# Optimization experiments

Measured on AMD Instinct MI355X. Metric: run time of the kernel, lower is better.

Reference implementation:

```python
import jax, jax.numpy as jnp
import numpy as np

BN_EPS = 1e-5


def scatter_mean(src, idx, num_segments):
    # torch_scatter scatter_mean: sum / clamp(count, min=1)
    s = jax.ops.segment_sum(src, idx, num_segments=num_segments)
    c = jax.ops.segment_sum(jnp.ones((src.shape[0],), src.dtype), idx, num_segments=num_segments)
    return s / jnp.maximum(c, 1.0)[:, None]


def batch_norm(h, gamma, beta):
    # BatchNorm1d with track_running_stats=False: always uses batch stats (biased var)
    mu = jnp.mean(h, axis=0, keepdims=True)
    var = jnp.mean((h - mu) ** 2, axis=0, keepdims=True)
    return (h - mu) * jax.lax.rsqrt(var + BN_EPS) * gamma + beta


def setup_inputs() -> dict:
    key = jax.random.key(0)
    ks = jax.random.split(key, 16)
    N, E, B, D = 50000, 800000, 256, 64
    x = jax.random.normal(ks[0], (N, D), dtype=jnp.float32)
    edge_attr = jax.random.normal(ks[1], (E, D), dtype=jnp.float32)
    u = jax.random.normal(ks[2], (B, D), dtype=jnp.float32)
    edge_index = jax.random.randint(ks[3], (2, E), 0, N, dtype=jnp.int64)
    batch = jnp.sort(jax.random.randint(ks[4], (N,), 0, B, dtype=jnp.int64))
    def lin_init(k, fan_in, fan_out):
        k1, k2 = jax.random.split(k)
        bound = 1.0 / np.sqrt(fan_in)
        W = jax.random.uniform(k1, (fan_out, fan_in), minval=-bound, maxval=bound, dtype=jnp.float32)
        b = jax.random.uniform(k2, (fan_out,), minval=-bound, maxval=bound, dtype=jnp.float32)
        return W, b
    W0, b0 = lin_init(ks[5], 3 * D, D)
    W1, b1 = lin_init(ks[6], D, D)
    W2, b2 = lin_init(ks[7], D, D)
    g0 = jnp.ones((D,), jnp.float32); be0 = jnp.zeros((D,), jnp.float32)
    g1 = jnp.ones((D,), jnp.float32); be1 = jnp.zeros((D,), jnp.float32)
    g2 = jnp.ones((D,), jnp.float32); be2 = jnp.zeros((D,), jnp.float32)
    return dict(x=x, edge_attr=edge_attr, u=u, edge_index=edge_index, batch=batch,
                W0=W0, b0=b0, W1=W1, b1=b1, W2=W2, b2=b2,
                g0=g0, be0=be0, g1=g1, be1=be1, g2=g2, be2=be2)


def reference(x, edge_attr, u, edge_index, batch,
              W0, b0, W1, b1, W2, b2, g0, be0, g1, be1, g2, be2):
    N = x.shape[0]
    B = u.shape[0]
    # edge -> node mean, then node -> graph mean
    u_e = scatter_mean(edge_attr, edge_index[0, :], N)   # [N, D]
    u_e = scatter_mean(u_e, batch, B)                    # [B, D]
    u_v = scatter_mean(x, batch, B)                      # [B, D]
    comb = jnp.concatenate([u_e, u_v, u], axis=1)        # [B, 3D]
    out = comb
    for (W, b, g, be) in ((W0, b0, g0, be0), (W1, b1, g1, be1), (W2, b2, g2, be2)):
        out = out @ W.T + b
        out = jax.nn.relu(out)
        out = batch_norm(out, g, be)
        # dropout is a no-op in eval mode
    return out
```

## Files before the change

kernel.cpp:

```cpp
#include <hip/hip_runtime.h>
#include <hip/hip_bf16.h>

#define DD 64
#define ECH 128
#define NEB 256
#define GB 256
#define MAXPER 3200

typedef __attribute__((ext_vector_type(8))) short bf16x8_t;
typedef __attribute__((ext_vector_type(4))) float f32x4_t;

__device__ __forceinline__ ushort f2b(float x) {
  __hip_bfloat16 h = __float2bfloat16(x);
  ushort r;
  __builtin_memcpy(&r, &h, 2);
  return r;
}

__device__ __forceinline__ uint swz(uint b) { return b ^ ((((b >> 8) & 7u)) << 4); }

__global__ __launch_bounds__(256) void k_zero(int* __restrict__ p, int n) {
  int gid = blockIdx.x * blockDim.x + threadIdx.x;
  int stride = gridDim.x * blockDim.x;
  for (int i = gid; i < n; i += stride) p[i] = 0;
}

__global__ __launch_bounds__(256) void k_hist(const int* __restrict__ eidx,
                                              int* __restrict__ cnt, int E) {
  int gid = blockIdx.x * blockDim.x + threadIdx.x;
  int stride = gridDim.x * blockDim.x;
  int E4 = E >> 2;
  const int4* e4 = reinterpret_cast<const int4*>(eidx);
  for (int i = gid; i < E4; i += stride) {
    int4 v = e4[i];
    atomicAdd(&cnt[v.x], 1);
    atomicAdd(&cnt[v.y], 1);
    atomicAdd(&cnt[v.z], 1);
    atomicAdd(&cnt[v.w], 1);
  }
  for (int e = (E4 << 2) + gid; e < E; e += stride) atomicAdd(&cnt[eidx[e]], 1);
}

__global__ __launch_bounds__(512) void k_edgesum(const float* __restrict__ edge_attr,
                                                 const int* __restrict__ eidx,
                                                 const int* __restrict__ cnt,
                                                 const int* __restrict__ batch,
                                                 float* __restrict__ partial, int E) {
  __shared__ ushort S[256 * 128];
  __shared__ ushort Vt[64 * 128];
  __shared__ int2 meta[MAXPER];
  const int tid = threadIdx.x;
  const int lane = tid & 63, wv = tid >> 6;
  const int r15 = lane & 15, kq = lane >> 4;

  const int per = (E + NEB - 1) / NEB;
  const int base = blockIdx.x * per;
  const int nE = max(0, min(per, E - base));
  const int nch = (nE + ECH - 1) / ECH;

  const int e0 = (tid >> 3) * 2;
  const int d0 = (tid & 7) * 8;

  float4 rA[4], rB[4];

#define LOADC(c, R)                                                              \
  do {                                                                           \
    size_t r0_ = (size_t)min(base + (c)*ECH + e0, E - 1);                        \
    size_t r1_ = (size_t)min(base + (c)*ECH + e0 + 1, E - 1);                    \
    const float4* p0_ = reinterpret_cast<const float4*>(edge_attr + r0_ * DD + d0); \
    const float4* p1_ = reinterpret_cast<const float4*>(edge_attr + r1_ * DD + d0); \
    R[0] = p0_[0];                                                               \
    R[1] = p0_[1];                                                               \
    R[2] = p1_[0];                                                               \
    R[3] = p1_[1];                                                               \
  } while (0)

#define PHASEW(c, R)                                                             \
  do {                                                                           \
    _Pragma("unroll") for (int q = 0; q < 2; ++q) {                              \
      _Pragma("unroll") for (int j = 0; j < 4; ++j) {                            \
        int d_ = d0 + q * 4 + j;                                                 \
        uint w32_ = (uint)f2b(((const float*)&R[q])[j]) |                        \
                    ((uint)f2b(((const float*)&R[2 + q])[j]) << 16);             \
        *(uint*)((char*)Vt + swz(((uint)d_ * 128 + e0) * 2)) = w32_;             \
      }                                                                          \
    }                                                                            \
    if (tid < ECH) {                                                             \
      if (prev >= 0) *(ushort*)((char*)S + swz(((uint)prev * 128 + tid) * 2)) = 0; \
      int2 mm_ = meta[(c)*ECH + tid];                                            \
      if (mm_.x >= 0) {                                                          \
        *(ushort*)((char*)S + swz(((uint)mm_.x * 128 + tid) * 2)) =              \
            f2b(__int_as_float(mm_.y));                                          \
        prev = mm_.x;                                                            \
      } else {                                                                   \
        prev = -1;                                                               \
      }                                                                          \
    }                                                                            \
  } while (0)

#define MFMAP()                                                                  \
  do {                                                                           \
    _Pragma("unroll") for (int ks = 0; ks < 4; ++ks) {                           \
      uint ko_ = (uint)(ks * 32 + kq * 8) * 2;                                   \
      bf16x8_t a0_ = *(const bf16x8_t*)((const char*)S +                         \
                                        swz((uint)(wv * 32 + r15) * 256 + ko_)); \
      bf16x8_t a1_ = *(const bf16x8_t*)((const char*)S +                         \
                                        swz((uint)(wv * 32 + 16 + r15) * 256 + ko_)); \
      bf16x8_t b0_ = *(const bf16x8_t*)((const char*)Vt + swz((uint)(r15)*256 + ko_)); \
      bf16x8_t b1_ = *(const bf16x8_t*)((const char*)Vt +                        \
                                        swz((uint)(16 + r15) * 256 + ko_));      \
      bf16x8_t b2_ = *(const bf16x8_t*)((const char*)Vt +                        \
                                        swz((uint)(32 + r15) * 256 + ko_));      \
      bf16x8_t b3_ = *(const bf16x8_t*)((const char*)Vt +                        \
                                        swz((uint)(48 + r15) * 256 + ko_));      \
      acc[0][0] = __builtin_amdgcn_mfma_f32_16x16x32_bf16(a0_, b0_, acc[0][0], 0, 0, 0); \
      acc[0][1] = __builtin_amdgcn_mfma_f32_16x16x32_bf16(a0_, b1_, acc[0][1], 0, 0, 0); \
      acc[0][2] = __builtin_amdgcn_mfma_f32_16x16x32_bf16(a0_, b2_, acc[0][2], 0, 0, 0); \
      acc[0][3] = __builtin_amdgcn_mfma_f32_16x16x32_bf16(a0_, b3_, acc[0][3], 0, 0, 0); \
      acc[1][0] = __builtin_amdgcn_mfma_f32_16x16x32_bf16(a1_, b0_, acc[1][0], 0, 0, 0); \
      acc[1][1] = __builtin_amdgcn_mfma_f32_16x16x32_bf16(a1_, b1_, acc[1][1], 0, 0, 0); \
      acc[1][2] = __builtin_amdgcn_mfma_f32_16x16x32_bf16(a1_, b2_, acc[1][2], 0, 0, 0); \
      acc[1][3] = __builtin_amdgcn_mfma_f32_16x16x32_bf16(a1_, b3_, acc[1][3], 0, 0, 0); \
    }                                                                            \
  } while (0)

#define LGKM0() asm volatile("s_waitcnt lgkmcnt(0)" ::: "memory")

  f32x4_t acc[2][4];
#pragma unroll
  for (int a = 0; a < 2; ++a)
#pragma unroll
    for (int nt = 0; nt < 4; ++nt) acc[a][nt] = (f32x4_t)(0.0f);

  LOADC(0, rA);
  if (nch > 1) LOADC(1, rB);
  for (int i = tid; i < 256 * 128 / 2; i += 512) ((uint*)S)[i] = 0u;
  for (int i = tid; i < MAXPER; i += 512) {
    int pb = -1;
    float pw = 0.f;
    if (i < nE) {
      int n = eidx[base + i];
      pw = 1.0f / fmaxf((float)cnt[n], 1.0f);
      pb = batch[n];
    }
    meta[i] = make_int2(pb, __float_as_int(pw));
  }
  int prev = -1;
  __syncthreads();

  for (int c = 0; c < nch; c += 2) {
    PHASEW(c, rA);
    LGKM0();
    __builtin_amdgcn_s_barrier();
    if (c + 2 < nch) LOADC(c + 2, rA);
    MFMAP();
    LGKM0();
    __builtin_amdgcn_s_barrier();
    if (c + 1 < nch) {
      PHASEW(c + 1, rB);
      LGKM0();
      __builtin_amdgcn_s_barrier();
      if (c + 3 < nch) LOADC(c + 3, rB);
      MFMAP();
      LGKM0();
      __builtin_amdgcn_s_barrier();
    }
  }

  float* outp = partial + (size_t)blockIdx.x * GB * DD;
#pragma unroll
  for (int a = 0; a < 2; ++a)
#pragma unroll
    for (int nt = 0; nt < 4; ++nt)
#pragma unroll
      for (int j = 0; j < 4; ++j) {
        int row = wv * 32 + a * 16 + kq * 4 + j;
        int col = nt * 16 + r15;
        outp[row * DD + col] = acc[a][nt][j];
      }
#undef LOADC
#undef PHASEW
#undef MFMAP
#undef LGKM0
}

__global__ __launch_bounds__(256) void k_reduce(const float* __restrict__ partial,
                                                const float* __restrict__ x,
                                                const float* __restrict__ u,
                                                const int* __restrict__ batch,
                                                ushort* __restrict__ comb, int N) {
  __shared__ int s_lo, s_hi;
  __shared__ float rE[4][64], rV[4][64];
  int b = blockIdx.x;
  int tid = threadIdx.x;
  if (tid == 0) {
    int lo = 0, hi = N;
    while (lo < hi) { int m = (lo + hi) >> 1; if (batch[m] < b) lo = m + 1; else hi = m; }
    s_lo = lo;
    hi = N;
    while (lo < hi) { int m = (lo + hi) >> 1; if (batch[m] < b + 1) lo = m + 1; else hi = m; }
    s_hi = lo;
  }
  __syncthreads();
  int lo = s_lo, hi = s_hi;
  int d = tid & 63, sub = tid >> 6;
  float accE = 0.f, accV = 0.f;
  for (int p = sub; p < NEB; p += 4)
    accE += partial[((size_t)p * GB + b) * DD + d];
  for (int n = lo + sub; n < hi; n += 4)
    accV += x[(size_t)n * DD + d];
  rE[sub][d] = accE;
  rV[sub][d] = accV;
  __syncthreads();
  if (sub == 0) {
    float invNb = 1.0f / fmaxf((float)(hi - lo), 1.0f);
    float ue = (rE[0][d] + rE[1][d] + rE[2][d] + rE[3][d]) * invNb;
    float uv = (rV[0][d] + rV[1][d] + rV[2][d] + rV[3][d]) * invNb;
    ushort* row = comb + (size_t)b * 192;
    row[d] = f2b(ue);
    row[64 + d] = f2b(uv);
    row[128 + d] = f2b(u[(size_t)b * DD + d]);
  }
}

template <int K, int WS, bool FIRST, bool LAST>
__device__ __forceinline__ void mlp_layer(int tid, const ushort* __restrict__ combg,
                                          float* hbuf, ushort* a_lds,
                                          const ushort* w_lds, const float* bias_s,
                                          float* ps, float* pq, float* ab, float* bb,
                                          const float* __restrict__ gamma,
                                          const float* __restrict__ beta,
                                          float* __restrict__ out) {
  const int lane = tid & 63, wv = tid >> 6;
  f32x4_t acc[2][4];
#pragma unroll
  for (int a = 0; a < 2; ++a)
#pragma unroll
    for (int nt = 0; nt < 4; ++nt) acc[a][nt] = (f32x4_t)(0.0f);

  const int m0 = wv * 32;
  const int r15 = lane & 15, kq = lane >> 4;
  for (int kk = 0; kk < K; kk += 32) {
    int koff = kk + kq * 8;
    bf16x8_t af[2], bf[4];
    if (FIRST) {
      const ushort* ap = combg + (size_t)(m0 + r15) * 192 + koff;
      af[0] = *reinterpret_cast<const bf16x8_t*>(ap);
      af[1] = *reinterpret_cast<const bf16x8_t*>(ap + 16 * 192);
    } else {
      const ushort* ap = &a_lds[(m0 + r15) * 72 + koff];
      af[0] = *reinterpret_cast<const bf16x8_t*>(ap);
      af[1] = *reinterpret_cast<const bf16x8_t*>(ap + 16 * 72);
    }
#pragma unroll
    for (int nt = 0; nt < 4; ++nt)
      bf[nt] = *reinterpret_cast<const bf16x8_t*>(&w_lds[(nt * 16 + r15) * WS + koff]);
#pragma unroll
    for (int a = 0; a < 2; ++a)
#pragma unroll
      for (int nt = 0; nt < 4; ++nt)
        acc[a][nt] = __builtin_amdgcn_mfma_f32_16x16x32_bf16(af[a], bf[nt], acc[a][nt], 0, 0, 0);
  }

#pragma unroll
  for (int a = 0; a < 2; ++a) {
#pragma unroll
    for (int nt = 0; nt < 4; ++nt) {
      int col = nt * 16 + r15;
#pragma unroll
      for (int j = 0; j < 4; ++j) {
        int row = m0 + a * 16 + kq * 4 + j;
        float v = acc[a][nt][j] + bias_s[col];
        hbuf[row * 65 + col] = fmaxf(v, 0.f);
      }
    }
  }
  __syncthreads();

  {
    int col = tid & 63, seg = tid >> 6;
    float s = 0.f, q = 0.f;
#pragma unroll
    for (int t = 0; t < 32; ++t) {
      float v = hbuf[(seg * 32 + t) * 65 + col];
      s += v;
      q += v * v;
    }
    ps[seg * 64 + col] = s;
    pq[seg * 64 + col] = q;
  }
  __syncthreads();
  if (tid < 64) {
    float s = 0.f, q = 0.f;
#pragma unroll
    for (int g = 0; g < 8; ++g) {
      s += ps[g * 64 + tid];
      q += pq[g * 64 + tid];
    }
    float mu = s * (1.0f / 256.0f);
    float var = q * (1.0f / 256.0f) - mu * mu;
    float rs = rsqrtf(var + 1e-5f);
    float A = gamma[tid] * rs;
    ab[tid] = A;
    bb[tid] = beta[tid] - mu * A;
  }
  __syncthreads();
  for (int i = tid; i < 256 * 64; i += 512) {
    int r = i >> 6, c = i & 63;
    float y = hbuf[r * 65 + c] * ab[c] + bb[c];
    if (LAST)
      out[i] = y;
    else
      a_lds[r * 72 + c] = f2b(y);
  }
  __syncthreads();
}

__global__ __launch_bounds__(512) void k_mlp(const ushort* __restrict__ comb,
                                             const float* W0, const float* b0,
                                             const float* W1, const float* b1,
                                             const float* W2, const float* b2,
                                             const float* g0, const float* be0,
                                             const float* g1, const float* be1,
                                             const float* g2, const float* be2,
                                             float* __restrict__ out) {
  __shared__ __align__(16) float hbuf[256 * 65];
  __shared__ __align__(16) ushort a_lds[256 * 72];
  __shared__ __align__(16) ushort w0s[64 * 200];
  __shared__ __align__(16) ushort w1s[64 * 72];
  __shared__ __align__(16) ushort w2s[64 * 72];
  __shared__ float ps[8 * 64], pq[8 * 64];
  __shared__ float b0s[64], b1s[64], b2s[64], ab[64], bb[64];
  int tid = threadIdx.x;

  for (int i = tid; i < 64 * 192; i += 512) {
    int r = i / 192, c = i - r * 192;
    w0s[r * 200 + c] = f2b(W0[i]);
  }
  for (int i = tid; i < 64 * 64; i += 512) {
    int r = i >> 6, c = i & 63;
    w1s[r * 72 + c] = f2b(W1[i]);
    w2s[r * 72 + c] = f2b(W2[i]);
  }
  if (tid < 64) {
    b0s[tid] = b0[tid];
    b1s[tid] = b1[tid];
    b2s[tid] = b2[tid];
  }
  __syncthreads();

  mlp_layer<192, 200, true, false>(tid, comb, hbuf, a_lds, w0s, b0s, ps, pq, ab, bb,
                                   g0, be0, nullptr);
  mlp_layer<64, 72, false, false>(tid, comb, hbuf, a_lds, w1s, b1s, ps, pq, ab, bb,
                                  g1, be1, nullptr);
  mlp_layer<64, 72, false, true>(tid, comb, hbuf, a_lds, w2s, b2s, ps, pq, ab, bb,
                                 g2, be2, out);
}

extern "C" void kernel_launch(void* const* d_in, const int* in_sizes, int n_in,
                              void* d_out, int out_size, void* d_ws, size_t ws_size,
                              hipStream_t stream) {
  (void)n_in; (void)out_size; (void)ws_size;
  const float* x         = (const float*)d_in[0];
  const float* edge_attr = (const float*)d_in[1];
  const float* u         = (const float*)d_in[2];
  const int*   eidx      = (const int*)d_in[3];
  const int*   batch     = (const int*)d_in[4];
  const float* W0 = (const float*)d_in[5];
  const float* b0 = (const float*)d_in[6];
  const float* W1 = (const float*)d_in[7];
  const float* b1 = (const float*)d_in[8];
  const float* W2 = (const float*)d_in[9];
  const float* b2 = (const float*)d_in[10];
  const float* g0 = (const float*)d_in[11];
  const float* be0 = (const float*)d_in[12];
  const float* g1 = (const float*)d_in[13];
  const float* be1 = (const float*)d_in[14];
  const float* g2 = (const float*)d_in[15];
  const float* be2 = (const float*)d_in[16];

  int N = in_sizes[0] / DD;
  int E = in_sizes[1] / DD;

  float* partial = (float*)d_ws;
  int* cnt = (int*)(partial + (size_t)NEB * GB * DD);
  ushort* comb = (ushort*)(cnt + ((N + 3) & ~3));

  k_zero<<<64, 256, 0, stream>>>(cnt, N);
  k_hist<<<1024, 256, 0, stream>>>(eidx, cnt, E);
  k_edgesum<<<NEB, 512, 0, stream>>>(edge_attr, eidx, cnt, batch, partial, E);
  k_reduce<<<256, 256, 0, stream>>>(partial, x, u, batch, comb, N);
  k_mlp<<<1, 512, 0, stream>>>(comb, W0, b0, W1, b1, W2, b2,
                               g0, be0, g1, be1, g2, be2, (float*)d_out);
}
```

Before: 143.0 us.

## Split MFMA K-dimension across wave halves and widen swizzle to cut LDS traffic

```diff
diff --git a/kernel.cpp b/kernel.cpp
--- a/kernel.cpp
+++ b/kernel.cpp
@@ -17,7 +17,9 @@
   return r;
 }
 
-__device__ __forceinline__ uint swz(uint b) { return b ^ ((((b >> 8) & 7u)) << 4); }
+__device__ __forceinline__ uint swz(uint b) {
+  return b ^ (((((b >> 8) & 7u)) ^ ((b >> 11) & 7u)) << 4);
+}
 
 __global__ __launch_bounds__(256) void k_zero(int* __restrict__ p, int n) {
   int gid = blockIdx.x * blockDim.x + threadIdx.x;
@@ -52,6 +54,8 @@
   const int tid = threadIdx.x;
   const int lane = tid & 63, wv = tid >> 6;
   const int r15 = lane & 15, kq = lane >> 4;
+  const int kh = wv >> 2;
+  const int mq = wv & 3;
 
   const int per = (E + NEB - 1) / NEB;
   const int base = blockIdx.x * per;
@@ -100,12 +104,8 @@
 
 #define MFMAP()                                                                  \
   do {                                                                           \
-    _Pragma("unroll") for (int ks = 0; ks < 4; ++ks) {                           \
-      uint ko_ = (uint)(ks * 32 + kq * 8) * 2;                                   \
-      bf16x8_t a0_ = *(const bf16x8_t*)((const char*)S +                         \
-                                        swz((uint)(wv * 32 + r15) * 256 + ko_)); \
-      bf16x8_t a1_ = *(const bf16x8_t*)((const char*)S +                         \
-                                        swz((uint)(wv * 32 + 16 + r15) * 256 + ko_)); \
+    _Pragma("unroll") for (int ks = 0; ks < 2; ++ks) {                           \
+      uint ko_ = (uint)((kh * 2 + ks) * 32 + kq * 8) * 2;                        \
       bf16x8_t b0_ = *(const bf16x8_t*)((const char*)Vt + swz((uint)(r15)*256 + ko_)); \
       bf16x8_t b1_ = *(const bf16x8_t*)((const char*)Vt +                        \
                                         swz((uint)(16 + r15) * 256 + ko_));      \
@@ -113,22 +113,22 @@
                                         swz((uint)(32 + r15) * 256 + ko_));      \
       bf16x8_t b3_ = *(const bf16x8_t*)((const char*)Vt +                        \
                                         swz((uint)(48 + r15) * 256 + ko_));      \
-      acc[0][0] = __builtin_amdgcn_mfma_f32_16x16x32_bf16(a0_, b0_, acc[0][0], 0, 0, 0); \
-      acc[0][1] = __builtin_amdgcn_mfma_f32_16x16x32_bf16(a0_, b1_, acc[0][1], 0, 0, 0); \
-      acc[0][2] = __builtin_amdgcn_mfma_f32_16x16x32_bf16(a0_, b2_, acc[0][2], 0, 0, 0); \
-      acc[0][3] = __builtin_amdgcn_mfma_f32_16x16x32_bf16(a0_, b3_, acc[0][3], 0, 0, 0); \
-      acc[1][0] = __builtin_amdgcn_mfma_f32_16x16x32_bf16(a1_, b0_, acc[1][0], 0, 0, 0); \
-      acc[1][1] = __builtin_amdgcn_mfma_f32_16x16x32_bf16(a1_, b1_, acc[1][1], 0, 0, 0); \
-      acc[1][2] = __builtin_amdgcn_mfma_f32_16x16x32_bf16(a1_, b2_, acc[1][2], 0, 0, 0); \
-      acc[1][3] = __builtin_amdgcn_mfma_f32_16x16x32_bf16(a1_, b3_, acc[1][3], 0, 0, 0); \
+      _Pragma("unroll") for (int mt = 0; mt < 4; ++mt) {                         \
+        bf16x8_t a_ = *(const bf16x8_t*)((const char*)S +                        \
+                                         swz((uint)(mq * 64 + mt * 16 + r15) * 256 + ko_)); \
+        acc[mt][0] = __builtin_amdgcn_mfma_f32_16x16x32_bf16(a_, b0_, acc[mt][0], 0, 0, 0); \
+        acc[mt][1] = __builtin_amdgcn_mfma_f32_16x16x32_bf16(a_, b1_, acc[mt][1], 0, 0, 0); \
+        acc[mt][2] = __builtin_amdgcn_mfma_f32_16x16x32_bf16(a_, b2_, acc[mt][2], 0, 0, 0); \
+        acc[mt][3] = __builtin_amdgcn_mfma_f32_16x16x32_bf16(a_, b3_, acc[mt][3], 0, 0, 0); \
+      }                                                                          \
     }                                                                            \
   } while (0)
 
 #define LGKM0() asm volatile("s_waitcnt lgkmcnt(0)" ::: "memory")
 
-  f32x4_t acc[2][4];
-#pragma unroll
-  for (int a = 0; a < 2; ++a)
+  f32x4_t acc[4][4];
+#pragma unroll
+  for (int a = 0; a < 4; ++a)
 #pragma unroll
     for (int nt = 0; nt < 4; ++nt) acc[a][nt] = (f32x4_t)(0.0f);
 
@@ -167,17 +167,30 @@
     }
   }
 
-  float* outp = partial + (size_t)blockIdx.x * GB * DD;
-#pragma unroll
-  for (int a = 0; a < 2; ++a)
-#pragma unroll
-    for (int nt = 0; nt < 4; ++nt)
-#pragma unroll
-      for (int j = 0; j < 4; ++j) {
-        int row = wv * 32 + a * 16 + kq * 4 + j;
-        int col = nt * 16 + r15;
-        outp[row * DD + col] = acc[a][nt][j];
-      }
+  __syncthreads();
+  float* Smrg = (float*)S;
+  if (kh == 0) {
+#pragma unroll
+    for (int mt = 0; mt < 4; ++mt)
+#pragma unroll
+      for (int nt = 0; nt < 4; ++nt)
+#pragma unroll
+        for (int j = 0; j < 4; ++j)
+          Smrg[(mq * 64 + mt * 16 + kq * 4 + j) * 64 + nt * 16 + r15] = acc[mt][nt][j];
+  }
+  __syncthreads();
+  if (kh == 1) {
+    float* outp = partial + (size_t)blockIdx.x * GB * DD;
+#pragma unroll
+    for (int mt = 0; mt < 4; ++mt)
+#pragma unroll
+      for (int nt = 0; nt < 4; ++nt)
+#pragma unroll
+        for (int j = 0; j < 4; ++j) {
+          int idx = (mq * 64 + mt * 16 + kq * 4 + j) * 64 + nt * 16 + r15;
+          outp[idx] = Smrg[idx] + acc[mt][nt][j];
+        }
+  }
 #undef LOADC
 #undef PHASEW
 #undef MFMAP
```

Measured after the change: 136.1 us, median of 2. 4.8% less time.

## Halve edge chunk size and double block count in edge-sum MFMA kernel

Applied to the files above, without the earlier changes.

```diff
diff --git a/kernel.cpp b/kernel.cpp
--- a/kernel.cpp
+++ b/kernel.cpp
@@ -2,10 +2,10 @@
 #include <hip/hip_bf16.h>
 
 #define DD 64
-#define ECH 128
-#define NEB 256
+#define ECH 64
+#define NEB 512
 #define GB 256
-#define MAXPER 3200
+#define MAXPER 1600
 
 typedef __attribute__((ext_vector_type(8))) short bf16x8_t;
 typedef __attribute__((ext_vector_type(4))) float f32x4_t;
@@ -17,7 +17,9 @@
   return r;
 }
 
-__device__ __forceinline__ uint swz(uint b) { return b ^ ((((b >> 8) & 7u)) << 4); }
+__device__ __forceinline__ uint swz128(uint b) {
+  return b ^ (((((b >> 7) & 7u)) ^ ((b >> 10) & 7u)) << 4);
+}
 
 __global__ __launch_bounds__(256) void k_zero(int* __restrict__ p, int n) {
   int gid = blockIdx.x * blockDim.x + threadIdx.x;
@@ -41,55 +43,49 @@
   for (int e = (E4 << 2) + gid; e < E; e += stride) atomicAdd(&cnt[eidx[e]], 1);
 }
 
-__global__ __launch_bounds__(512) void k_edgesum(const float* __restrict__ edge_attr,
-                                                 const int* __restrict__ eidx,
-                                                 const int* __restrict__ cnt,
-                                                 const int* __restrict__ batch,
-                                                 float* __restrict__ partial, int E) {
-  __shared__ ushort S[256 * 128];
-  __shared__ ushort Vt[64 * 128];
+__global__ __launch_bounds__(512, 4) void k_edgesum(const float* __restrict__ edge_attr,
+                                                    const int* __restrict__ eidx,
+                                                    const int* __restrict__ cnt,
+                                                    const int* __restrict__ batch,
+                                                    float* __restrict__ partial, int E) {
+  __shared__ ushort S[256 * 64];
+  __shared__ ushort Vt[64 * 64];
   __shared__ int2 meta[MAXPER];
   const int tid = threadIdx.x;
   const int lane = tid & 63, wv = tid >> 6;
   const int r15 = lane & 15, kq = lane >> 4;
+  const int m0 = wv * 32;
 
   const int per = (E + NEB - 1) / NEB;
   const int base = blockIdx.x * per;
   const int nE = max(0, min(per, E - base));
   const int nch = (nE + ECH - 1) / ECH;
 
-  const int e0 = (tid >> 3) * 2;
-  const int d0 = (tid & 7) * 8;
-
-  float4 rA[4], rB[4];
+  const int p = tid & 31;
+  const int d0 = (tid >> 5) * 4;
+
+  float4 rA[2], rB[2];
 
 #define LOADC(c, R)                                                              \
   do {                                                                           \
-    size_t r0_ = (size_t)min(base + (c)*ECH + e0, E - 1);                        \
-    size_t r1_ = (size_t)min(base + (c)*ECH + e0 + 1, E - 1);                    \
-    const float4* p0_ = reinterpret_cast<const float4*>(edge_attr + r0_ * DD + d0); \
-    const float4* p1_ = reinterpret_cast<const float4*>(edge_attr + r1_ * DD + d0); \
-    R[0] = p0_[0];                                                               \
-    R[1] = p0_[1];                                                               \
-    R[2] = p1_[0];                                                               \
-    R[3] = p1_[1];                                                               \
+    size_t r0_ = (size_t)min(base + (c)*ECH + 2 * p, E - 1);                     \
+    size_t r1_ = (size_t)min(base + (c)*ECH + 2 * p + 1, E - 1);                 \
+    R[0] = *reinterpret_cast<const float4*>(edge_attr + r0_ * DD + d0);          \
+    R[1] = *reinterpret_cast<const float4*>(edge_attr + r1_ * DD + d0);          \
   } while (0)
 
 #define PHASEW(c, R)                                                             \
   do {                                                                           \
-    _Pragma("unroll") for (int q = 0; q < 2; ++q) {                              \
-      _Pragma("unroll") for (int j = 0; j < 4; ++j) {                            \
-        int d_ = d0 + q * 4 + j;                                                 \
-        uint w32_ = (uint)f2b(((const float*)&R[q])[j]) |                        \
-                    ((uint)f2b(((const float*)&R[2 + q])[j]) << 16);             \
-        *(uint*)((char*)Vt + swz(((uint)d_ * 128 + e0) * 2)) = w32_;             \
-      }                                                                          \
+    _Pragma("unroll") for (int j = 0; j < 4; ++j) {                              \
+      uint w32_ = (uint)f2b(((const float*)&R[0])[j]) |                          \
+                  ((uint)f2b(((const float*)&R[1])[j]) << 16);                   \
+      *(uint*)((char*)Vt + swz128(((uint)(d0 + j)) * 128 + (uint)p * 4)) = w32_; \
     }                                                                            \
     if (tid < ECH) {                                                             \
-      if (prev >= 0) *(ushort*)((char*)S + swz(((uint)prev * 128 + tid) * 2)) = 0; \
+      if (prev >= 0) *(ushort*)((char*)S + swz128((uint)prev * 128 + tid * 2)) = 0; \
       int2 mm_ = meta[(c)*ECH + tid];                                            \
       if (mm_.x >= 0) {                                                          \
-        *(ushort*)((char*)S + swz(((uint)mm_.x * 128 + tid) * 2)) =              \
+        *(ushort*)((char*)S + swz128((uint)mm_.x * 128 + tid * 2)) =             \
             f2b(__int_as_float(mm_.y));                                          \
         prev = mm_.x;                                                            \
       } else {                                                                   \
@@ -100,27 +96,23 @@
 
 #define MFMAP()                                                                  \
   do {                                                                           \
-    _Pragma("unroll") for (int ks = 0; ks < 4; ++ks) {                           \
-      uint ko_ = (uint)(ks * 32 + kq * 8) * 2;                                   \
-      bf16x8_t a0_ = *(const bf16x8_t*)((const char*)S +                         \
-                                        swz((uint)(wv * 32 + r15) * 256 + ko_)); \
-      bf16x8_t a1_ = *(const bf16x8_t*)((const char*)S +                         \
-                                        swz((uint)(wv * 32 + 16 + r15) * 256 + ko_)); \
-      bf16x8_t b0_ = *(const bf16x8_t*)((const char*)Vt + swz((uint)(r15)*256 + ko_)); \
+    _Pragma("unroll") for (int ks = 0; ks < 2; ++ks) {                           \
+      uint ko_ = (uint)(ks * 64 + kq * 16);                                      \
+      bf16x8_t b0_ = *(const bf16x8_t*)((const char*)Vt + swz128((uint)(r15)*128 + ko_)); \
       bf16x8_t b1_ = *(const bf16x8_t*)((const char*)Vt +                        \
-                                        swz((uint)(16 + r15) * 256 + ko_));      \
+                                        swz128((uint)(16 + r15) * 128 + ko_));   \
       bf16x8_t b2_ = *(const bf16x8_t*)((const char*)Vt +                        \
-                                        swz((uint)(32 + r15) * 256 + ko_));      \
+                                        swz128((uint)(32 + r15) * 128 + ko_));   \
       bf16x8_t b3_ = *(const bf16x8_t*)((const char*)Vt +                        \
-                                        swz((uint)(48 + r15) * 256 + ko_));      \
-      acc[0][0] = __builtin_amdgcn_mfma_f32_16x16x32_bf16(a0_, b0_, acc[0][0], 0, 0, 0); \
-      acc[0][1] = __builtin_amdgcn_mfma_f32_16x16x32_bf16(a0_, b1_, acc[0][1], 0, 0, 0); \
-      acc[0][2] = __builtin_amdgcn_mfma_f32_16x16x32_bf16(a0_, b2_, acc[0][2], 0, 0, 0); \
-      acc[0][3] = __builtin_amdgcn_mfma_f32_16x16x32_bf16(a0_, b3_, acc[0][3], 0, 0, 0); \
-      acc[1][0] = __builtin_amdgcn_mfma_f32_16x16x32_bf16(a1_, b0_, acc[1][0], 0, 0, 0); \
-      acc[1][1] = __builtin_amdgcn_mfma_f32_16x16x32_bf16(a1_, b1_, acc[1][1], 0, 0, 0); \
-      acc[1][2] = __builtin_amdgcn_mfma_f32_16x16x32_bf16(a1_, b2_, acc[1][2], 0, 0, 0); \
-      acc[1][3] = __builtin_amdgcn_mfma_f32_16x16x32_bf16(a1_, b3_, acc[1][3], 0, 0, 0); \
+                                        swz128((uint)(48 + r15) * 128 + ko_));   \
+      _Pragma("unroll") for (int mt = 0; mt < 2; ++mt) {                         \
+        bf16x8_t a_ = *(const bf16x8_t*)((const char*)S +                        \
+                                         swz128((uint)(m0 + mt * 16 + r15) * 128 + ko_)); \
+        acc[mt][0] = __builtin_amdgcn_mfma_f32_16x16x32_bf16(a_, b0_, acc[mt][0], 0, 0, 0); \
+        acc[mt][1] = __builtin_amdgcn_mfma_f32_16x16x32_bf16(a_, b1_, acc[mt][1], 0, 0, 0); \
+        acc[mt][2] = __builtin_amdgcn_mfma_f32_16x16x32_bf16(a_, b2_, acc[mt][2], 0, 0, 0); \
+        acc[mt][3] = __builtin_amdgcn_mfma_f32_16x16x32_bf16(a_, b3_, acc[mt][3], 0, 0, 0); \
+      }                                                                          \
     }                                                                            \
   } while (0)
 
@@ -132,9 +124,9 @@
 #pragma unroll
     for (int nt = 0; nt < 4; ++nt) acc[a][nt] = (f32x4_t)(0.0f);
 
-  LOADC(0, rA);
+  if (nch > 0) LOADC(0, rA);
   if (nch > 1) LOADC(1, rB);
-  for (int i = tid; i < 256 * 128 / 2; i += 512) ((uint*)S)[i] = 0u;
+  for (int i = tid; i < 256 * 64 / 2; i += 512) ((uint*)S)[i] = 0u;
   for (int i = tid; i < MAXPER; i += 512) {
     int pb = -1;
     float pw = 0.f;
@@ -169,14 +161,14 @@
 
   float* outp = partial + (size_t)blockIdx.x * GB * DD;
 #pragma unroll
-  for (int a = 0; a < 2; ++a)
+  for (int mt = 0; mt < 2; ++mt)
 #pragma unroll
     for (int nt = 0; nt < 4; ++nt)
 #pragma unroll
       for (int j = 0; j < 4; ++j) {
-        int row = wv * 32 + a * 16 + kq * 4 + j;
+        int row = m0 + mt * 16 + kq * 4 + j;
         int col = nt * 16 + r15;
-        outp[row * DD + col] = acc[a][nt][j];
+        outp[row * DD + col] = acc[mt][nt][j];
       }
 #undef LOADC
 #undef PHASEW
```

Measured after the change: 163.0 us. +14.0%, slower.

## Precompute packed edge metadata in separate kernel and double edgesum grid

Applied to the files above, without the earlier changes.

```diff
diff --git a/kernel.cpp b/kernel.cpp
--- a/kernel.cpp
+++ b/kernel.cpp
@@ -3,9 +3,8 @@
 
 #define DD 64
 #define ECH 128
-#define NEB 256
+#define NEB 512
 #define GB 256
-#define MAXPER 3200
 
 typedef __attribute__((ext_vector_type(8))) short bf16x8_t;
 typedef __attribute__((ext_vector_type(4))) float f32x4_t;
@@ -17,7 +16,9 @@
   return r;
 }
 
-__device__ __forceinline__ uint swz(uint b) { return b ^ ((((b >> 8) & 7u)) << 4); }
+__device__ __forceinline__ uint swz(uint b) {
+  return b ^ (((((b >> 8) & 7u)) ^ ((b >> 11) & 7u)) << 4);
+}
 
 __global__ __launch_bounds__(256) void k_zero(int* __restrict__ p, int n) {
   int gid = blockIdx.x * blockDim.x + threadIdx.x;
@@ -41,17 +42,29 @@
   for (int e = (E4 << 2) + gid; e < E; e += stride) atomicAdd(&cnt[eidx[e]], 1);
 }
 
-__global__ __launch_bounds__(512) void k_edgesum(const float* __restrict__ edge_attr,
-                                                 const int* __restrict__ eidx,
-                                                 const int* __restrict__ cnt,
-                                                 const int* __restrict__ batch,
-                                                 float* __restrict__ partial, int E) {
-  __shared__ ushort S[256 * 128];
-  __shared__ ushort Vt[64 * 128];
-  __shared__ int2 meta[MAXPER];
+__global__ __launch_bounds__(256) void k_meta(const int* __restrict__ eidx,
+                                              const int* __restrict__ cnt,
+                                              const int* __restrict__ batch,
+                                              uint* __restrict__ umeta, int E) {
+  int gid = blockIdx.x * blockDim.x + threadIdx.x;
+  int stride = gridDim.x * blockDim.x;
+  for (int e = gid; e < E; e += stride) {
+    int n = eidx[e];
+    float w = 1.0f / fmaxf((float)cnt[n], 1.0f);
+    umeta[e] = (uint)f2b(w) | ((uint)batch[n] << 16);
+  }
+}
+
+__global__ __launch_bounds__(512, 4) void k_edgesum(const float* __restrict__ edge_attr,
+                                                    const uint* __restrict__ umeta,
+                                                    float* __restrict__ partial, int E) {
+  extern __shared__ __align__(16) char smem[];
+  ushort* S = (ushort*)smem;
+  ushort* Vt = (ushort*)(smem + 65536);
   const int tid = threadIdx.x;
   const int lane = tid & 63, wv = tid >> 6;
   const int r15 = lane & 15, kq = lane >> 4;
+  const int m0 = wv * 32;
 
   const int per = (E + NEB - 1) / NEB;
   const int base = blockIdx.x * per;
@@ -62,8 +75,9 @@
   const int d0 = (tid & 7) * 8;
 
   float4 rA[4], rB[4];
-
-#define LOADC(c, R)                                                              \
+  uint mA = 0, mB = 0;
+
+#define LOADC(c, R, M)                                                           \
   do {                                                                           \
     size_t r0_ = (size_t)min(base + (c)*ECH + e0, E - 1);                        \
     size_t r1_ = (size_t)min(base + (c)*ECH + e0 + 1, E - 1);                    \
@@ -73,9 +87,10 @@
     R[1] = p0_[1];                                                               \
     R[2] = p1_[0];                                                               \
     R[3] = p1_[1];                                                               \
+    if (tid < ECH) M = umeta[min(base + (c)*ECH + tid, E - 1)];                  \
   } while (0)
 
-#define PHASEW(c, R)                                                             \
+#define PHASEW(c, R, M)                                                          \
   do {                                                                           \
     _Pragma("unroll") for (int q = 0; q < 2; ++q) {                              \
       _Pragma("unroll") for (int j = 0; j < 4; ++j) {                            \
@@ -87,11 +102,10 @@
     }                                                                            \
     if (tid < ECH) {                                                             \
       if (prev >= 0) *(ushort*)((char*)S + swz(((uint)prev * 128 + tid) * 2)) = 0; \
-      int2 mm_ = meta[(c)*ECH + tid];                                            \
-      if (mm_.x >= 0) {                                                          \
-        *(ushort*)((char*)S + swz(((uint)mm_.x * 128 + tid) * 2)) =              \
-            f2b(__int_as_float(mm_.y));                                          \
-        prev = mm_.x;                                                            \
+      if ((c)*ECH + tid < nE) {                                                  \
+        int b_ = (int)(M >> 16);                                                 \
+        *(ushort*)((char*)S + swz(((uint)b_ * 128 + tid) * 2)) = (ushort)(M & 0xffffu); \
+        prev = b_;                                                               \
       } else {                                                                   \
         prev = -1;                                                               \
       }                                                                          \
@@ -102,10 +116,6 @@
   do {                                                                           \
     _Pragma("unroll") for (int ks = 0; ks < 4; ++ks) {                           \
       uint ko_ = (uint)(ks * 32 + kq * 8) * 2;                                   \
-      bf16x8_t a0_ = *(const bf16x8_t*)((const char*)S +                         \
-                                        swz((uint)(wv * 32 + r15) * 256 + ko_)); \
-      bf16x8_t a1_ = *(const bf16x8_t*)((const char*)S +                         \
-                                        swz((uint)(wv * 32 + 16 + r15) * 256 + ko_)); \
       bf16x8_t b0_ = *(const bf16x8_t*)((const char*)Vt + swz((uint)(r15)*256 + ko_)); \
       bf16x8_t b1_ = *(const bf16x8_t*)((const char*)Vt +                        \
                                         swz((uint)(16 + r15) * 256 + ko_));      \
@@ -113,14 +123,14 @@
                                         swz((uint)(32 + r15) * 256 + ko_));      \
       bf16x8_t b3_ = *(const bf16x8_t*)((const char*)Vt +                        \
                                         swz((uint)(48 + r15) * 256 + ko_));      \
-      acc[0][0] = __builtin_amdgcn_mfma_f32_16x16x32_bf16(a0_, b0_, acc[0][0], 0, 0, 0); \
-      acc[0][1] = __builtin_amdgcn_mfma_f32_16x16x32_bf16(a0_, b1_, acc[0][1], 0, 0, 0); \
-      acc[0][2] = __builtin_amdgcn_mfma_f32_16x16x32_bf16(a0_, b2_, acc[0][2], 0, 0, 0); \
-      acc[0][3] = __builtin_amdgcn_mfma_f32_16x16x32_bf16(a0_, b3_, acc[0][3], 0, 0, 0); \
-      acc[1][0] = __builtin_amdgcn_mfma_f32_16x16x32_bf16(a1_, b0_, acc[1][0], 0, 0, 0); \
-      acc[1][1] = __builtin_amdgcn_mfma_f32_16x16x32_bf16(a1_, b1_, acc[1][1], 0, 0, 0); \
-      acc[1][2] = __builtin_amdgcn_mfma_f32_16x16x32_bf16(a1_, b2_, acc[1][2], 0, 0, 0); \
-      acc[1][3] = __builtin_amdgcn_mfma_f32_16x16x32_bf16(a1_, b3_, acc[1][3], 0, 0, 0); \
+      _Pragma("unroll") for (int mt = 0; mt < 2; ++mt) {                         \
+        bf16x8_t a_ = *(const bf16x8_t*)((const char*)S +                        \
+                                         swz((uint)(m0 + mt * 16 + r15) * 256 + ko_)); \
+        acc[mt][0] = __builtin_amdgcn_mfma_f32_16x16x32_bf16(a_, b0_, acc[mt][0], 0, 0, 0); \
+        acc[mt][1] = __builtin_amdgcn_mfma_f32_16x16x32_bf16(a_, b1_, acc[mt][1], 0, 0, 0); \
+        acc[mt][2] = __builtin_amdgcn_mfma_f32_16x16x32_bf16(a_, b2_, acc[mt][2], 0, 0, 0); \
+        acc[mt][3] = __builtin_amdgcn_mfma_f32_16x16x32_bf16(a_, b3_, acc[mt][3], 0, 0, 0); \
+      }                                                                          \
     }                                                                            \
   } while (0)
 
@@ -132,35 +142,25 @@
 #pragma unroll
     for (int nt = 0; nt < 4; ++nt) acc[a][nt] = (f32x4_t)(0.0f);
 
-  LOADC(0, rA);
-  if (nch > 1) LOADC(1, rB);
+  if (nch > 0) LOADC(0, rA, mA);
+  if (nch > 1) LOADC(1, rB, mB);
   for (int i = tid; i < 256 * 128 / 2; i += 512) ((uint*)S)[i] = 0u;
-  for (int i = tid; i < MAXPER; i += 512) {
-    int pb = -1;
-    float pw = 0.f;
-    if (i < nE) {
-      int n = eidx[base + i];
-      pw = 1.0f / fmaxf((float)cnt[n], 1.0f);
-      pb = batch[n];
-    }
-    meta[i] = make_int2(pb, __float_as_int(pw));
-  }
   int prev = -1;
   __syncthreads();
 
   for (int c = 0; c < nch; c += 2) {
-    PHASEW(c, rA);
+    PHASEW(c, rA, mA);
     LGKM0();
     __builtin_amdgcn_s_barrier();
-    if (c + 2 < nch) LOADC(c + 2, rA);
+    if (c + 2 < nch) LOADC(c + 2, rA, mA);
     MFMAP();
     LGKM0();
     __builtin_amdgcn_s_barrier();
     if (c + 1 < nch) {
-      PHASEW(c + 1, rB);
+      PHASEW(c + 1, rB, mB);
       LGKM0();
       __builtin_amdgcn_s_barrier();
-      if (c + 3 < nch) LOADC(c + 3, rB);
+      if (c + 3 < nch) LOADC(c + 3, rB, mB);
       MFMAP();
       LGKM0();
       __builtin_amdgcn_s_barrier();
@@ -169,14 +169,14 @@
 
   float* outp = partial + (size_t)blockIdx.x * GB * DD;
 #pragma unroll
-  for (int a = 0; a < 2; ++a)
+  for (int mt = 0; mt < 2; ++mt)
 #pragma unroll
     for (int nt = 0; nt < 4; ++nt)
 #pragma unroll
       for (int j = 0; j < 4; ++j) {
-        int row = wv * 32 + a * 16 + kq * 4 + j;
+        int row = m0 + mt * 16 + kq * 4 + j;
         int col = nt * 16 + r15;
-        outp[row * DD + col] = acc[a][nt][j];
+        outp[row * DD + col] = acc[mt][nt][j];
       }
 #undef LOADC
 #undef PHASEW
@@ -384,11 +384,13 @@
 
   float* partial = (float*)d_ws;
   int* cnt = (int*)(partial + (size_t)NEB * GB * DD);
-  ushort* comb = (ushort*)(cnt + ((N + 3) & ~3));
+  uint* umeta = (uint*)(cnt + ((N + 3) & ~3));
+  ushort* comb = (ushort*)(umeta + ((E + 3) & ~3));
 
   k_zero<<<64, 256, 0, stream>>>(cnt, N);
   k_hist<<<1024, 256, 0, stream>>>(eidx, cnt, E);
-  k_edgesum<<<NEB, 512, 0, stream>>>(edge_attr, eidx, cnt, batch, partial, E);
+  k_meta<<<2048, 256, 0, stream>>>(eidx, cnt, batch, umeta, E);
+  k_edgesum<<<NEB, 512, 81920, stream>>>(edge_attr, umeta, partial, E);
   k_reduce<<<256, 256, 0, stream>>>(partial, x, u, batch, comb, N);
   k_mlp<<<1, 512, 0, stream>>>(comb, W0, b0, W1, b1, W2, b2,
                                g0, be0, g1, be1, g2, be2, (float*)d_out);
```

New measurement: 166.5 us. +16.5%, slower.
